# Optimization experiments

Measured on AMD Instinct MI355X. Metric: run time of the kernel, lower is better.

Reference implementation:

```python
import jax, jax.numpy as jnp
import numpy as np

N_NODES = 100000
N_EDGES = 1600000
IN_CH, HID_CH, OUT_CH = 128, 64, 64


def setup_inputs() -> dict:
    key = jax.random.key(0)
    ks = jax.random.split(key, 9)
    def glorot(k, shape):
        lim = jnp.sqrt(6.0 / (shape[0] + shape[1]))
        return jax.random.uniform(k, shape, jnp.float32, -lim, lim)
    return {
        "x": jax.random.normal(ks[0], (N_NODES, IN_CH), jnp.float32),
        "edge_src": jax.random.randint(ks[1], (N_EDGES,), 0, N_NODES, jnp.int32),
        "edge_dst": jax.random.randint(ks[2], (N_EDGES,), 0, N_NODES, jnp.int32),
        "W1": glorot(ks[3], (IN_CH, HID_CH)),
        "b1": jnp.zeros((HID_CH,), jnp.float32),
        "W2": glorot(ks[4], (HID_CH, HID_CH)),
        "b2": jnp.zeros((HID_CH,), jnp.float32),
        "W3": glorot(ks[5], (HID_CH, OUT_CH)),
        "b3": jnp.zeros((OUT_CH,), jnp.float32),
    }


def _gcn_layer(h, W, b, edge_src, edge_dst):
    # GCNConv(normalize=False): transform then sum-aggregate over incoming edges
    hw = h @ W                                   # [N, d_out]
    msg = hw[edge_src]                           # [E, d_out] gather
    agg = jax.ops.segment_sum(msg, edge_dst, num_segments=N_NODES)  # scatter-add
    return agg + b


def reference(x, edge_src, edge_dst, W1, b1, W2, b2, W3, b3):
    # layer 1 + relu (dropout is identity at inference)
    h = jax.nn.relu(_gcn_layer(x, W1, b1, edge_src, edge_dst))
    # layer 2 + relu
    h = jax.nn.relu(_gcn_layer(h, W2, b2, edge_src, edge_dst))
    # final layer, no activation
    return _gcn_layer(h, W3, b3, edge_src, edge_dst)
```

## Files before the change

### kernel.cpp

```cpp
#include <hip/hip_runtime.h>

#define CH 64
#define BNODES 128
#define NB_MAX 1024
#define CUR_PAD 16
#define SCAT_CHUNK 8192
#define SCAT_THREADS 1024
#define BSLACK 1024

typedef unsigned short ushort_t;
typedef unsigned int uint_t;
typedef short short8_t __attribute__((ext_vector_type(8)));
typedef float float4_t __attribute__((ext_vector_type(4)));

static __device__ __forceinline__ ushort_t f2bf(float x) {
    uint_t u = __float_as_uint(x);
    u = (u + 0x7FFFu + ((u >> 16) & 1u)) >> 16;
    return (ushort_t)u;
}
static __device__ __forceinline__ float bf2f(ushort_t s) {
    return __uint_as_float((uint_t)s << 16);
}

__global__ __launch_bounds__(256) void wt_kernel(
    const float* __restrict__ W, ushort_t* __restrict__ Wt, int K)
{
    for (int i = threadIdx.x; i < K * CH; i += 256) {
        int n = i / K, k = i % K;
        Wt[i] = f2bf(W[(size_t)k * CH + n]);
    }
}

template<int K, typename T>
__global__ __launch_bounds__(256) void gemm_mfma(
    const T* __restrict__ h, const ushort_t* __restrict__ Wt,
    ushort_t* __restrict__ outb, int n)
{
    constexpr int LDH = K + 8;
    constexpr int C8  = K / 8;
    constexpr int KC  = K / 32;
    __shared__ ushort_t Hs[128 * LDH];

    const int t    = threadIdx.x;
    const int lane = t & 63;
    const int wv   = t >> 6;
    const int l15  = lane & 15;
    const int quad = lane >> 4;
    const int row0 = blockIdx.x * 128;

    short8_t bfrag[4][KC];
    #pragma unroll
    for (int nt = 0; nt < 4; ++nt)
        #pragma unroll
        for (int kc = 0; kc < KC; ++kc)
            bfrag[nt][kc] = *(const short8_t*)(Wt + (size_t)(nt * 16 + l15) * K + kc * 32 + quad * 8);

    for (int idx = t; idx < 128 * C8; idx += 256) {
        int r  = idx / C8;
        int c8 = idx % C8;
        int rg = row0 + r;
        short8_t v = (short8_t)0;
        if (rg < n) {
            if constexpr (sizeof(T) == 4) {
                const float* p = (const float*)h + (size_t)rg * K + c8 * 8;
                float4 f0 = *(const float4*)p;
                float4 f1 = *(const float4*)(p + 4);
                v[0] = (short)f2bf(f0.x); v[1] = (short)f2bf(f0.y);
                v[2] = (short)f2bf(f0.z); v[3] = (short)f2bf(f0.w);
                v[4] = (short)f2bf(f1.x); v[5] = (short)f2bf(f1.y);
                v[6] = (short)f2bf(f1.z); v[7] = (short)f2bf(f1.w);
            } else {
                v = *(const short8_t*)((const ushort_t*)h + (size_t)rg * K + c8 * 8);
            }
        }
        *(short8_t*)&Hs[r * LDH + c8 * 8] = v;
    }
    __syncthreads();

    float4_t acc[2][4];
    #pragma unroll
    for (int mi = 0; mi < 2; ++mi)
        #pragma unroll
        for (int nt = 0; nt < 4; ++nt)
            acc[mi][nt] = (float4_t)0.f;

    #pragma unroll
    for (int kc = 0; kc < KC; ++kc) {
        short8_t a0 = *(const short8_t*)&Hs[(wv * 32 +      l15) * LDH + kc * 32 + quad * 8];
        short8_t a1 = *(const short8_t*)&Hs[(wv * 32 + 16 + l15) * LDH + kc * 32 + quad * 8];
        #pragma unroll
        for (int nt = 0; nt < 4; ++nt) {
            acc[0][nt] = __builtin_amdgcn_mfma_f32_16x16x32_bf16(a0, bfrag[nt][kc], acc[0][nt], 0, 0, 0);
            acc[1][nt] = __builtin_amdgcn_mfma_f32_16x16x32_bf16(a1, bfrag[nt][kc], acc[1][nt], 0, 0, 0);
        }
    }

    #pragma unroll
    for (int mi = 0; mi < 2; ++mi) {
        #pragma unroll
        for (int r = 0; r < 4; ++r) {
            int row = row0 + wv * 32 + mi * 16 + quad * 4 + r;
            if (row <= n) {
                #pragma unroll
                for (int nt = 0; nt < 4; ++nt)
                    outb[(size_t)row * CH + nt * 16 + l15] = f2bf(acc[mi][nt][r]);
            }
        }
    }
}

__global__ __launch_bounds__(256) void bucket_hist(
    const int* __restrict__ dst, int* __restrict__ bcnt, int E, int NB)
{
    __shared__ int h[NB_MAX];
    for (int i = threadIdx.x; i < NB; i += 256) h[i] = 0;
    __syncthreads();
    for (int i = blockIdx.x * 256 + threadIdx.x; i < E; i += gridDim.x * 256)
        atomicAdd(&h[dst[i] >> 7], 1);
    __syncthreads();
    for (int i = threadIdx.x; i < NB; i += 256) {
        int v = h[i];
        if (v) atomicAdd(&bcnt[i], v);
    }
}

__global__ __launch_bounds__(256) void bucket_scan(
    const int* __restrict__ bcnt, int* __restrict__ boff,
    int* __restrict__ cursor, int NB)
{
    __shared__ int tsum[256];
    int t = threadIdx.x;
    int base = t * 4;
    int c[4];
    #pragma unroll
    for (int j = 0; j < 4; ++j) {
        int i = base + j;
        c[j] = (i < NB) ? bcnt[i] : 0;
    }
    int local = c[0] + c[1] + c[2] + c[3];
    tsum[t] = local;
    __syncthreads();
    for (int off = 1; off < 256; off <<= 1) {
        int v = (t >= off) ? tsum[t - off] : 0;
        __syncthreads();
        tsum[t] += v;
        __syncthreads();
    }
    int p = tsum[t] - local;
    #pragma unroll
    for (int j = 0; j < 4; ++j) {
        int i = base + j;
        if (i < NB) { boff[i] = p; cursor[i * CUR_PAD] = p; }
        p += c[j];
    }
    if (t == 255) boff[NB] = tsum[255];
}

__global__ __launch_bounds__(SCAT_THREADS) void bucket_scatter_blk(
    const int* __restrict__ src, const int* __restrict__ dst,
    int* __restrict__ cursor, int* __restrict__ bucketed, int E, int NB)
{
    __shared__ int hist[NB_MAX];
    __shared__ int rbase[NB_MAX];
    __shared__ int lcur[NB_MAX];

    const int t = threadIdx.x;
    const int s = blockIdx.x * SCAT_CHUNK;
    const int e = min(s + SCAT_CHUNK, E);

    for (int i = t; i < NB; i += SCAT_THREADS) hist[i] = 0;
    __syncthreads();

    for (int i = s + t; i < e; i += SCAT_THREADS)
        atomicAdd(&hist[dst[i] >> 7], 1);
    __syncthreads();

    for (int i = t; i < NB; i += SCAT_THREADS) {
        int c = hist[i];
        rbase[i] = c ? atomicAdd(&cursor[i * CUR_PAD], c) : 0;
        lcur[i] = 0;
    }
    __syncthreads();

    for (int i = s + t; i < e; i += SCAT_THREADS) {
        int d = dst[i];
        int b = d >> 7;
        int p = atomicAdd(&lcur[b], 1);
        bucketed[rbase[b] + p] = ((d & 127) << 17) | src[i];
    }
}

__global__ __launch_bounds__(256) void node_sort(
    const int* __restrict__ bucketed, const int* __restrict__ boff,
    int* __restrict__ sorted_src, int2* __restrict__ seg, int N, int zrow)
{
    __shared__ int cnt[BNODES];
    __shared__ int sc[BNODES];
    __shared__ int cur[BNODES];
    const int bk = blockIdx.x;
    const int t  = threadIdx.x;
    const int s  = boff[bk];
    const int e  = boff[bk + 1];
    const int sbase = (s + bk * BSLACK + 7) & ~7;

    if (t < BNODES) cnt[t] = 0;
    __syncthreads();
    for (int i = s + t; i < e; i += 256)
        atomicAdd(&cnt[((unsigned)bucketed[i]) >> 17], 1);
    __syncthreads();

    int pc = 0;
    if (t < BNODES) { pc = (cnt[t] + 7) & ~7; sc[t] = pc; }
    __syncthreads();
    for (int o = 1; o < BNODES; o <<= 1) {
        int v = (t < BNODES && t >= o) ? sc[t - o] : 0;
        __syncthreads();
        if (t < BNODES) sc[t] += v;
        __syncthreads();
    }
    if (t < BNODES) {
        int pexcl = sc[t] - pc;
        cur[t] = pexcl;
        int node = bk * BNODES + t;
        if (node < N) seg[node] = make_int2(sbase + pexcl, pc);
        for (int k = cnt[t]; k < pc; ++k)
            sorted_src[sbase + pexcl + k] = zrow;
    }
    __syncthreads();

    for (int i = s + t; i < e; i += 256) {
        int p = bucketed[i];
        int d = ((unsigned)p) >> 17;
        int pos = atomicAdd(&cur[d], 1);
        sorted_src[sbase + pos] = p & 0x1FFFF;
    }
}

template<bool BF16_RELU_OUT>
__global__ __launch_bounds__(256) void aggregate_kernel(
    const ushort_t* __restrict__ hwb, const int* __restrict__ sorted_src,
    const int2* __restrict__ seg, const float* __restrict__ bias,
    ushort_t* __restrict__ outb, float* __restrict__ outf, int N)
{
    const int lane = threadIdx.x & 63;
    const int node = blockIdx.x * 4 + (threadIdx.x >> 6);
    if (node >= N) return;

    int2 sc   = seg[node];
    int  base = __builtin_amdgcn_readfirstlane(sc.x);
    int  pc   = __builtin_amdgcn_readfirstlane(sc.y);

    const int4* sp4 = (const int4*)(sorted_src + base);

    float a0 = bias[lane], a1 = 0.f, a2 = 0.f, a3 = 0.f;
    float a4 = 0.f, a5 = 0.f, a6 = 0.f, a7 = 0.f;

    int u = 0;
    for (; u + 16 <= pc; u += 16) {
        int4 q0 = sp4[(u >> 2) + 0];
        int4 q1 = sp4[(u >> 2) + 1];
        int4 q2 = sp4[(u >> 2) + 2];
        int4 q3 = sp4[(u >> 2) + 3];
        int i0  = __builtin_amdgcn_readfirstlane(q0.x);
        int i1  = __builtin_amdgcn_readfirstlane(q0.y);
        int i2  = __builtin_amdgcn_readfirstlane(q0.z);
        int i3  = __builtin_amdgcn_readfirstlane(q0.w);
        int i4  = __builtin_amdgcn_readfirstlane(q1.x);
        int i5  = __builtin_amdgcn_readfirstlane(q1.y);
        int i6  = __builtin_amdgcn_readfirstlane(q1.z);
        int i7  = __builtin_amdgcn_readfirstlane(q1.w);
        int i8  = __builtin_amdgcn_readfirstlane(q2.x);
        int i9  = __builtin_amdgcn_readfirstlane(q2.y);
        int i10 = __builtin_amdgcn_readfirstlane(q2.z);
        int i11 = __builtin_amdgcn_readfirstlane(q2.w);
        int i12 = __builtin_amdgcn_readfirstlane(q3.x);
        int i13 = __builtin_amdgcn_readfirstlane(q3.y);
        int i14 = __builtin_amdgcn_readfirstlane(q3.z);
        int i15 = __builtin_amdgcn_readfirstlane(q3.w);
        ushort_t v0  = hwb[(size_t)i0  * CH + lane];
        ushort_t v1  = hwb[(size_t)i1  * CH + lane];
        ushort_t v2  = hwb[(size_t)i2  * CH + lane];
        ushort_t v3  = hwb[(size_t)i3  * CH + lane];
        ushort_t v4  = hwb[(size_t)i4  * CH + lane];
        ushort_t v5  = hwb[(size_t)i5  * CH + lane];
        ushort_t v6  = hwb[(size_t)i6  * CH + lane];
        ushort_t v7  = hwb[(size_t)i7  * CH + lane];
        ushort_t v8  = hwb[(size_t)i8  * CH + lane];
        ushort_t v9  = hwb[(size_t)i9  * CH + lane];
        ushort_t v10 = hwb[(size_t)i10 * CH + lane];
        ushort_t v11 = hwb[(size_t)i11 * CH + lane];
        ushort_t v12 = hwb[(size_t)i12 * CH + lane];
        ushort_t v13 = hwb[(size_t)i13 * CH + lane];
        ushort_t v14 = hwb[(size_t)i14 * CH + lane];
        ushort_t v15 = hwb[(size_t)i15 * CH + lane];
        a0 += bf2f(v0);  a1 += bf2f(v1);  a2 += bf2f(v2);  a3 += bf2f(v3);
        a4 += bf2f(v4);  a5 += bf2f(v5);  a6 += bf2f(v6);  a7 += bf2f(v7);
        a0 += bf2f(v8);  a1 += bf2f(v9);  a2 += bf2f(v10); a3 += bf2f(v11);
        a4 += bf2f(v12); a5 += bf2f(v13); a6 += bf2f(v14); a7 += bf2f(v15);
    }
    for (; u < pc; u += 8) {
        int4 qa = sp4[(u >> 2) + 0];
        int4 qb = sp4[(u >> 2) + 1];
        int i0 = __builtin_amdgcn_readfirstlane(qa.x);
        int i1 = __builtin_amdgcn_readfirstlane(qa.y);
        int i2 = __builtin_amdgcn_readfirstlane(qa.z);
        int i3 = __builtin_amdgcn_readfirstlane(qa.w);
        int i4 = __builtin_amdgcn_readfirstlane(qb.x);
        int i5 = __builtin_amdgcn_readfirstlane(qb.y);
        int i6 = __builtin_amdgcn_readfirstlane(qb.z);
        int i7 = __builtin_amdgcn_readfirstlane(qb.w);
        ushort_t v0 = hwb[(size_t)i0 * CH + lane];
        ushort_t v1 = hwb[(size_t)i1 * CH + lane];
        ushort_t v2 = hwb[(size_t)i2 * CH + lane];
        ushort_t v3 = hwb[(size_t)i3 * CH + lane];
        ushort_t v4 = hwb[(size_t)i4 * CH + lane];
        ushort_t v5 = hwb[(size_t)i5 * CH + lane];
        ushort_t v6 = hwb[(size_t)i6 * CH + lane];
        ushort_t v7 = hwb[(size_t)i7 * CH + lane];
        a0 += bf2f(v0); a1 += bf2f(v1); a2 += bf2f(v2); a3 += bf2f(v3);
        a4 += bf2f(v4); a5 += bf2f(v5); a6 += bf2f(v6); a7 += bf2f(v7);
    }

    float r = ((a0 + a1) + (a2 + a3)) + ((a4 + a5) + (a6 + a7));
    if (BF16_RELU_OUT) {
        outb[(size_t)node * CH + lane] = f2bf(fmaxf(r, 0.f));
    } else {
        outf[(size_t)node * CH + lane] = r;
    }
}

extern "C" void kernel_launch(void* const* d_in, const int* in_sizes, int n_in,
                              void* d_out, int out_size, void* d_ws, size_t ws_size,
                              hipStream_t stream) {
    const float* x    = (const float*)d_in[0];
    const int*   esrc = (const int*)  d_in[1];
    const int*   edst = (const int*)  d_in[2];
    const float* W1   = (const float*)d_in[3];
    const float* b1   = (const float*)d_in[4];
    const float* W2   = (const float*)d_in[5];
    const float* b2   = (const float*)d_in[6];
    const float* W3   = (const float*)d_in[7];
    const float* b3   = (const float*)d_in[8];
    float* out = (float*)d_out;

    const int N  = in_sizes[0] / 128;
    const int E  = in_sizes[1];
    const int NB = (N + BNODES - 1) / BNODES;

    char* ws = (char*)d_ws;
    ushort_t* hwb   = (ushort_t*)ws; ws += (size_t)(N + 1) * CH * 2;
    ushort_t* hb    = (ushort_t*)ws; ws += (size_t)N * CH * 2;
    int* bucketed   = (int*)ws;      ws += (size_t)E * 4;
    ws = (char*)(((uintptr_t)ws + 15) & ~(uintptr_t)15);
    int* sorted_src = (int*)ws;      ws += ((size_t)E + (size_t)NB * BSLACK + 64) * 4;
    int2* seg       = (int2*)ws;     ws += (size_t)N * 8;
    int* bcnt       = (int*)ws;      ws += (size_t)NB * 4;
    int* boff       = (int*)ws;      ws += (size_t)(NB + 1) * 4;
    ws = (char*)(((uintptr_t)ws + 63) & ~(uintptr_t)63);
    int* cursor     = (int*)ws;      ws += (size_t)NB * CUR_PAD * 4;
    ws = (char*)(((uintptr_t)ws + 15) & ~(uintptr_t)15);
    ushort_t* Wt1   = (ushort_t*)ws; ws += (size_t)CH * 128 * 2;
    ushort_t* Wt2   = (ushort_t*)ws; ws += (size_t)CH * 64 * 2;
    ushort_t* Wt3   = (ushort_t*)ws; ws += (size_t)CH * 64 * 2;

    dim3 blk(256);
    int gemmGrid = (N + 1 + 127) / 128;
    int aggGrid  = (N + 3) / 4;
    int scatGrid = (E + SCAT_CHUNK - 1) / SCAT_CHUNK;

    wt_kernel<<<1, blk, 0, stream>>>(W1, Wt1, 128);
    wt_kernel<<<1, blk, 0, stream>>>(W2, Wt2, 64);
    wt_kernel<<<1, blk, 0, stream>>>(W3, Wt3, 64);

    hipMemsetAsync(bcnt, 0, (size_t)NB * 4, stream);
    bucket_hist<<<256, blk, 0, stream>>>(edst, bcnt, E, NB);
    bucket_scan<<<1, blk, 0, stream>>>(bcnt, boff, cursor, NB);
    bucket_scatter_blk<<<scatGrid, dim3(SCAT_THREADS), 0, stream>>>(esrc, edst, cursor, bucketed, E, NB);
    node_sort<<<NB, blk, 0, stream>>>(bucketed, boff, sorted_src, seg, N, N );

    gemm_mfma<128, float><<<gemmGrid, blk, 0, stream>>>(x, Wt1, hwb, N);
    aggregate_kernel<true><<<aggGrid, blk, 0, stream>>>(hwb, sorted_src, seg, b1, hb, nullptr, N);
    gemm_mfma<64, ushort_t><<<gemmGrid, blk, 0, stream>>>(hb, Wt2, hwb, N);
    aggregate_kernel<true><<<aggGrid, blk, 0, stream>>>(hwb, sorted_src, seg, b2, hb, nullptr, N);
    gemm_mfma<64, ushort_t><<<gemmGrid, blk, 0, stream>>>(hb, Wt3, hwb, N);
    aggregate_kernel<false><<<aggGrid, blk, 0, stream>>>(hwb, sorted_src, seg, b3, nullptr, out, N);
}
```

Baseline: 309.2 us.

## Fuse prep launches, co-schedule histogram with first GEMM, vectorize aggregation gathers

Merges the three weight-transpose launches and the bucket-count memset into one prep kernel. The first GEMM and the edge histogram now run in a single launch using disjoint blocks, so they overlap and one launch is dropped. The aggregation kernel is reorganized so each wave handles four edges at a time: sixteen lanes each load 8 bytes (four bf16 channels) per row, using pre-scaled row offsets stored in sorted_src, and the partial sums are reduced across lane groups with shuffles. This trades per-lane scalar index broadcasts and 2-byte loads for wider loads plus a cross-lane reduction.

Result: no change. 309.8 us (+0.2%).

```diff
diff --git a/kernel.cpp b/kernel.cpp
--- a/kernel.cpp
+++ b/kernel.cpp
@@ -7,6 +7,7 @@
 #define SCAT_CHUNK 8192
 #define SCAT_THREADS 1024
 #define BSLACK 1024
+#define HIST_BLOCKS 256
 
 typedef unsigned short ushort_t;
 typedef unsigned int uint_t;
@@ -18,13 +19,26 @@
     u = (u + 0x7FFFu + ((u >> 16) & 1u)) >> 16;
     return (ushort_t)u;
 }
-static __device__ __forceinline__ float bf2f(ushort_t s) {
-    return __uint_as_float((uint_t)s << 16);
-}
-
-__global__ __launch_bounds__(256) void wt_kernel(
-    const float* __restrict__ W, ushort_t* __restrict__ Wt, int K)
-{
+static __device__ __forceinline__ float bflo(uint_t u) {
+    return __uint_as_float(u << 16);
+}
+static __device__ __forceinline__ float bfhi(uint_t u) {
+    return __uint_as_float(u & 0xFFFF0000u);
+}
+
+__global__ __launch_bounds__(256) void prep_kernel(
+    const float* __restrict__ W1, const float* __restrict__ W2, const float* __restrict__ W3,
+    ushort_t* __restrict__ Wt1, ushort_t* __restrict__ Wt2, ushort_t* __restrict__ Wt3,
+    int* __restrict__ bcnt, int NB)
+{
+    const int b = blockIdx.x;
+    if (b == 3) {
+        for (int i = threadIdx.x; i < NB; i += 256) bcnt[i] = 0;
+        return;
+    }
+    const float* W = (b == 0) ? W1 : (b == 1) ? W2 : W3;
+    ushort_t* Wt   = (b == 0) ? Wt1 : (b == 1) ? Wt2 : Wt3;
+    const int K    = (b == 0) ? 128 : 64;
     for (int i = threadIdx.x; i < K * CH; i += 256) {
         int n = i / K, k = i % K;
         Wt[i] = f2bf(W[(size_t)k * CH + n]);
@@ -32,21 +46,20 @@
 }
 
 template<int K, typename T>
-__global__ __launch_bounds__(256) void gemm_mfma(
+static __device__ __forceinline__ void gemm_body(
     const T* __restrict__ h, const ushort_t* __restrict__ Wt,
-    ushort_t* __restrict__ outb, int n)
+    ushort_t* __restrict__ outb, int n, ushort_t* Hs, int blockRow)
 {
     constexpr int LDH = K + 8;
     constexpr int C8  = K / 8;
     constexpr int KC  = K / 32;
-    __shared__ ushort_t Hs[128 * LDH];
 
     const int t    = threadIdx.x;
     const int lane = t & 63;
     const int wv   = t >> 6;
     const int l15  = lane & 15;
     const int quad = lane >> 4;
-    const int row0 = blockIdx.x * 128;
+    const int row0 = blockRow * 128;
 
     short8_t bfrag[4][KC];
     #pragma unroll
@@ -109,19 +122,36 @@
     }
 }
 
-__global__ __launch_bounds__(256) void bucket_hist(
-    const int* __restrict__ dst, int* __restrict__ bcnt, int E, int NB)
-{
-    __shared__ int h[NB_MAX];
-    for (int i = threadIdx.x; i < NB; i += 256) h[i] = 0;
-    __syncthreads();
-    for (int i = blockIdx.x * 256 + threadIdx.x; i < E; i += gridDim.x * 256)
-        atomicAdd(&h[dst[i] >> 7], 1);
-    __syncthreads();
-    for (int i = threadIdx.x; i < NB; i += 256) {
-        int v = h[i];
-        if (v) atomicAdd(&bcnt[i], v);
-    }
+template<int K, typename T>
+__global__ __launch_bounds__(256) void gemm_mfma(
+    const T* __restrict__ h, const ushort_t* __restrict__ Wt,
+    ushort_t* __restrict__ outb, int n)
+{
+    __shared__ ushort_t Hs[128 * (K + 8)];
+    gemm_body<K, T>(h, Wt, outb, n, Hs, blockIdx.x);
+}
+
+__global__ __launch_bounds__(256) void gemm1_hist(
+    const float* __restrict__ x, const ushort_t* __restrict__ Wt1,
+    ushort_t* __restrict__ outb, int n,
+    const int* __restrict__ dst, int* __restrict__ bcnt, int E, int NB, int gemmGrid)
+{
+    __shared__ ushort_t Hs[128 * 136];
+    if (blockIdx.x >= gemmGrid) {
+        int* h = (int*)Hs;
+        const int t = threadIdx.x;
+        for (int i = t; i < NB; i += 256) h[i] = 0;
+        __syncthreads();
+        for (int i = (blockIdx.x - gemmGrid) * 256 + t; i < E; i += HIST_BLOCKS * 256)
+            atomicAdd(&h[dst[i] >> 7], 1);
+        __syncthreads();
+        for (int i = t; i < NB; i += 256) {
+            int v = h[i];
+            if (v) atomicAdd(&bcnt[i], v);
+        }
+        return;
+    }
+    gemm_body<128, float>(x, Wt1, outb, n, Hs, blockIdx.x);
 }
 
 __global__ __launch_bounds__(256) void bucket_scan(
@@ -224,7 +254,7 @@
         int node = bk * BNODES + t;
         if (node < N) seg[node] = make_int2(sbase + pexcl, pc);
         for (int k = cnt[t]; k < pc; ++k)
-            sorted_src[sbase + pexcl + k] = zrow;
+            sorted_src[sbase + pexcl + k] = zrow << 4;
     }
     __syncthreads();
 
@@ -232,7 +262,7 @@
         int p = bucketed[i];
         int d = ((unsigned)p) >> 17;
         int pos = atomicAdd(&cur[d], 1);
-        sorted_src[sbase + pos] = p & 0x1FFFF;
+        sorted_src[sbase + pos] = (p & 0x1FFFF) << 4;
     }
 }
 
@@ -242,90 +272,62 @@
     const int2* __restrict__ seg, const float* __restrict__ bias,
     ushort_t* __restrict__ outb, float* __restrict__ outf, int N)
 {
-    const int lane = threadIdx.x & 63;
-    const int node = blockIdx.x * 4 + (threadIdx.x >> 6);
+    const int t    = threadIdx.x;
+    const int lane = t & 63;
+    const int node = blockIdx.x * 4 + (t >> 6);
     if (node >= N) return;
 
-    int2 sc   = seg[node];
-    int  base = __builtin_amdgcn_readfirstlane(sc.x);
-    int  pc   = __builtin_amdgcn_readfirstlane(sc.y);
-
-    const int4* sp4 = (const int4*)(sorted_src + base);
-
-    float a0 = bias[lane], a1 = 0.f, a2 = 0.f, a3 = 0.f;
-    float a4 = 0.f, a5 = 0.f, a6 = 0.f, a7 = 0.f;
+    int2 scv  = seg[node];
+    int  base = __builtin_amdgcn_readfirstlane(scv.x);
+    int  pc   = __builtin_amdgcn_readfirstlane(scv.y);
+
+    const int g = lane >> 4;
+    const int c = lane & 15;
+    const uint2* hw2 = (const uint2*)hwb;
+    const int*   sp  = sorted_src + base;
+
+    float a0 = 0.f, a1 = 0.f, a2 = 0.f, a3 = 0.f;
 
     int u = 0;
     for (; u + 16 <= pc; u += 16) {
-        int4 q0 = sp4[(u >> 2) + 0];
-        int4 q1 = sp4[(u >> 2) + 1];
-        int4 q2 = sp4[(u >> 2) + 2];
-        int4 q3 = sp4[(u >> 2) + 3];
-        int i0  = __builtin_amdgcn_readfirstlane(q0.x);
-        int i1  = __builtin_amdgcn_readfirstlane(q0.y);
-        int i2  = __builtin_amdgcn_readfirstlane(q0.z);
-        int i3  = __builtin_amdgcn_readfirstlane(q0.w);
-        int i4  = __builtin_amdgcn_readfirstlane(q1.x);
-        int i5  = __builtin_amdgcn_readfirstlane(q1.y);
-        int i6  = __builtin_amdgcn_readfirstlane(q1.z);
-        int i7  = __builtin_amdgcn_readfirstlane(q1.w);
-        int i8  = __builtin_amdgcn_readfirstlane(q2.x);
-        int i9  = __builtin_amdgcn_readfirstlane(q2.y);
-        int i10 = __builtin_amdgcn_readfirstlane(q2.z);
-        int i11 = __builtin_amdgcn_readfirstlane(q2.w);
-        int i12 = __builtin_amdgcn_readfirstlane(q3.x);
-        int i13 = __builtin_amdgcn_readfirstlane(q3.y);
-        int i14 = __builtin_amdgcn_readfirstlane(q3.z);
-        int i15 = __builtin_amdgcn_readfirstlane(q3.w);
-        ushort_t v0  = hwb[(size_t)i0  * CH + lane];
-        ushort_t v1  = hwb[(size_t)i1  * CH + lane];
-        ushort_t v2  = hwb[(size_t)i2  * CH + lane];
-        ushort_t v3  = hwb[(size_t)i3  * CH + lane];
-        ushort_t v4  = hwb[(size_t)i4  * CH + lane];
-        ushort_t v5  = hwb[(size_t)i5  * CH + lane];
-        ushort_t v6  = hwb[(size_t)i6  * CH + lane];
-        ushort_t v7  = hwb[(size_t)i7  * CH + lane];
-        ushort_t v8  = hwb[(size_t)i8  * CH + lane];
-        ushort_t v9  = hwb[(size_t)i9  * CH + lane];
-        ushort_t v10 = hwb[(size_t)i10 * CH + lane];
-        ushort_t v11 = hwb[(size_t)i11 * CH + lane];
-        ushort_t v12 = hwb[(size_t)i12 * CH + lane];
-        ushort_t v13 = hwb[(size_t)i13 * CH + lane];
-        ushort_t v14 = hwb[(size_t)i14 * CH + lane];
-        ushort_t v15 = hwb[(size_t)i15 * CH + lane];
-        a0 += bf2f(v0);  a1 += bf2f(v1);  a2 += bf2f(v2);  a3 += bf2f(v3);
-        a4 += bf2f(v4);  a5 += bf2f(v5);  a6 += bf2f(v6);  a7 += bf2f(v7);
-        a0 += bf2f(v8);  a1 += bf2f(v9);  a2 += bf2f(v10); a3 += bf2f(v11);
-        a4 += bf2f(v12); a5 += bf2f(v13); a6 += bf2f(v14); a7 += bf2f(v15);
-    }
-    for (; u < pc; u += 8) {
-        int4 qa = sp4[(u >> 2) + 0];
-        int4 qb = sp4[(u >> 2) + 1];
-        int i0 = __builtin_amdgcn_readfirstlane(qa.x);
-        int i1 = __builtin_amdgcn_readfirstlane(qa.y);
-        int i2 = __builtin_amdgcn_readfirstlane(qa.z);
-        int i3 = __builtin_amdgcn_readfirstlane(qa.w);
-        int i4 = __builtin_amdgcn_readfirstlane(qb.x);
-        int i5 = __builtin_amdgcn_readfirstlane(qb.y);
-        int i6 = __builtin_amdgcn_readfirstlane(qb.z);
-        int i7 = __builtin_amdgcn_readfirstlane(qb.w);
-        ushort_t v0 = hwb[(size_t)i0 * CH + lane];
-        ushort_t v1 = hwb[(size_t)i1 * CH + lane];
-        ushort_t v2 = hwb[(size_t)i2 * CH + lane];
-        ushort_t v3 = hwb[(size_t)i3 * CH + lane];
-        ushort_t v4 = hwb[(size_t)i4 * CH + lane];
-        ushort_t v5 = hwb[(size_t)i5 * CH + lane];
-        ushort_t v6 = hwb[(size_t)i6 * CH + lane];
-        ushort_t v7 = hwb[(size_t)i7 * CH + lane];
-        a0 += bf2f(v0); a1 += bf2f(v1); a2 += bf2f(v2); a3 += bf2f(v3);
-        a4 += bf2f(v4); a5 += bf2f(v5); a6 += bf2f(v6); a7 += bf2f(v7);
-    }
-
-    float r = ((a0 + a1) + (a2 + a3)) + ((a4 + a5) + (a6 + a7));
-    if (BF16_RELU_OUT) {
-        outb[(size_t)node * CH + lane] = f2bf(fmaxf(r, 0.f));
-    } else {
-        outf[(size_t)node * CH + lane] = r;
+        int r0 = sp[u +      g];
+        int r1 = sp[u +  4 + g];
+        int r2 = sp[u +  8 + g];
+        int r3 = sp[u + 12 + g];
+        uint2 v0 = hw2[(size_t)(r0 + c)];
+        uint2 v1 = hw2[(size_t)(r1 + c)];
+        uint2 v2 = hw2[(size_t)(r2 + c)];
+        uint2 v3 = hw2[(size_t)(r3 + c)];
+        a0 += bflo(v0.x); a1 += bfhi(v0.x); a2 += bflo(v0.y); a3 += bfhi(v0.y);
+        a0 += bflo(v1.x); a1 += bfhi(v1.x); a2 += bflo(v1.y); a3 += bfhi(v1.y);
+        a0 += bflo(v2.x); a1 += bfhi(v2.x); a2 += bflo(v2.y); a3 += bfhi(v2.y);
+        a0 += bflo(v3.x); a1 += bfhi(v3.x); a2 += bflo(v3.y); a3 += bfhi(v3.y);
+    }
+    if (u < pc) {
+        int r0 = sp[u +     g];
+        int r1 = sp[u + 4 + g];
+        uint2 v0 = hw2[(size_t)(r0 + c)];
+        uint2 v1 = hw2[(size_t)(r1 + c)];
+        a0 += bflo(v0.x); a1 += bfhi(v0.x); a2 += bflo(v0.y); a3 += bfhi(v0.y);
+        a0 += bflo(v1.x); a1 += bfhi(v1.x); a2 += bflo(v1.y); a3 += bfhi(v1.y);
+    }
+
+    a0 += __shfl_xor(a0, 16); a1 += __shfl_xor(a1, 16);
+    a2 += __shfl_xor(a2, 16); a3 += __shfl_xor(a3, 16);
+    a0 += __shfl_xor(a0, 32); a1 += __shfl_xor(a1, 32);
+    a2 += __shfl_xor(a2, 32); a3 += __shfl_xor(a3, 32);
+
+    float4 bv = *(const float4*)(bias + 4 * c);
+    a0 += bv.x; a1 += bv.y; a2 += bv.z; a3 += bv.w;
+
+    if (lane < 16) {
+        if (BF16_RELU_OUT) {
+            uint_t lo = (uint_t)f2bf(fmaxf(a0, 0.f)) | ((uint_t)f2bf(fmaxf(a1, 0.f)) << 16);
+            uint_t hi = (uint_t)f2bf(fmaxf(a2, 0.f)) | ((uint_t)f2bf(fmaxf(a3, 0.f)) << 16);
+            ((uint2*)outb)[(size_t)node * 16 + c] = make_uint2(lo, hi);
+        } else {
+            *(float4*)(outf + (size_t)node * CH + 4 * c) = make_float4(a0, a1, a2, a3);
+        }
     }
 }
 
@@ -368,17 +370,15 @@
     int aggGrid  = (N + 3) / 4;
     int scatGrid = (E + SCAT_CHUNK - 1) / SCAT_CHUNK;
 
-    wt_kernel<<<1, blk, 0, stream>>>(W1, Wt1, 128);
-    wt_kernel<<<1, blk, 0, stream>>>(W2, Wt2, 64);
-    wt_kernel<<<1, blk, 0, stream>>>(W3, Wt3, 64);
-
-    hipMemsetAsync(bcnt, 0, (size_t)NB * 4, stream);
-    bucket_hist<<<256, blk, 0, stream>>>(edst, bcnt, E, NB);
+    prep_kernel<<<4, blk, 0, stream>>>(W1, W2, W3, Wt1, Wt2, Wt3, bcnt, NB);
+
+    gemm1_hist<<<gemmGrid + HIST_BLOCKS, blk, 0, stream>>>(
+        x, Wt1, hwb, N, edst, bcnt, E, NB, gemmGrid);
+
     bucket_scan<<<1, blk, 0, stream>>>(bcnt, boff, cursor, NB);
     bucket_scatter_blk<<<scatGrid, dim3(SCAT_THREADS), 0, stream>>>(esrc, edst, cursor, bucketed, E, NB);
     node_sort<<<NB, blk, 0, stream>>>(bucketed, boff, sorted_src, seg, N, N );
 
-    gemm_mfma<128, float><<<gemmGrid, blk, 0, stream>>>(x, Wt1, hwb, N);
     aggregate_kernel<true><<<aggGrid, blk, 0, stream>>>(hwb, sorted_src, seg, b1, hb, nullptr, N);
     gemm_mfma<64, ushort_t><<<gemmGrid, blk, 0, stream>>>(hb, Wt2, hwb, N);
     aggregate_kernel<true><<<aggGrid, blk, 0, stream>>>(hwb, sorted_src, seg, b2, hb, nullptr, N);
```
